# Kernel optimization log

Hardware: AMD Instinct MI355X
Metric: run time of the kernel (lower is better)

## Reference

```python
import jax, jax.numpy as jnp
import numpy as np

B, S, D_MODEL = 2, 2048, 1024
H, D = 16, 64
D_INNER = H * D
EPS = 1e-5


def setup_inputs() -> dict:
    key = jax.random.key(0)
    ks = jax.random.split(key, 10)
    sc = 0.02
    return {
        "x": jax.random.normal(ks[0], (B, S, D_MODEL), dtype=jnp.float32),
        "Wq": jax.random.normal(ks[1], (D_MODEL, D_INNER), dtype=jnp.float32) * sc,
        "Wk": jax.random.normal(ks[2], (D_MODEL, D_INNER), dtype=jnp.float32) * sc,
        "Wv": jax.random.normal(ks[3], (D_MODEL, D_INNER), dtype=jnp.float32) * sc,
        "Wg": jax.random.normal(ks[4], (D_MODEL, D_INNER), dtype=jnp.float32) * sc,
        "Wa": jax.random.normal(ks[5], (D_MODEL, H), dtype=jnp.float32) * sc,
        "ba": jax.random.normal(ks[6], (H,), dtype=jnp.float32) * sc,
        "Wo": jax.random.normal(ks[7], (D_INNER, D_MODEL), dtype=jnp.float32) * sc,
        "gn_w": jnp.ones((D_INNER,), dtype=jnp.float32),
        "gn_b": jnp.zeros((D_INNER,), dtype=jnp.float32),
    }


def reference(x, Wq, Wk, Wv, Wg, Wa, ba, Wo, gn_w, gn_b):
    b, s, _ = x.shape
    # projections -> [B,H,S,D]
    q = jax.nn.silu(jnp.einsum('bsm,md->bsd', x, Wq).reshape(b, s, H, D).transpose(0, 2, 1, 3))
    k = jax.nn.silu(jnp.einsum('bsm,md->bsd', x, Wk).reshape(b, s, H, D).transpose(0, 2, 1, 3))
    v = jnp.einsum('bsm,md->bsd', x, Wv).reshape(b, s, H, D).transpose(0, 2, 1, 3)

    # data-dependent log forget gate, per head: [B,H,S]
    log_alpha = -jax.nn.softplus(jnp.einsum('bsm,mh->bsh', x, Wa) + ba)
    cum = jnp.cumsum(log_alpha, axis=1).transpose(0, 2, 1)  # [B,H,S]

    # decay[b,h,i,j] = exp(cum[i] - cum[j]) for j <= i, else 0
    diff = cum[:, :, :, None] - cum[:, :, None, :]  # [B,H,S,S]
    causal = jnp.tril(jnp.ones((s, s), dtype=bool))
    decay = jnp.exp(jnp.where(causal, diff, -jnp.inf))

    attn = jnp.einsum('bhid,bhjd->bhij', q, k) * decay
    o = jnp.einsum('bhij,bhjd->bhid', attn, v)  # [B,H,S,D]
    o = o.transpose(0, 2, 1, 3)  # [B,S,H,D]

    # GroupNorm(H groups) over channels-within-group and spatial dim S
    mean = jnp.mean(o, axis=(1, 3), keepdims=True)          # per (b,h)
    var = jnp.var(o, axis=(1, 3), keepdims=True)
    o = (o - mean) / jnp.sqrt(var + EPS)
    o = o * gn_w.reshape(H, D) + gn_b.reshape(H, D)
    o = o.reshape(b, s, H * D)

    gate = jax.nn.sigmoid(jnp.einsum('bsm,md->bsd', x, Wg))
    return jnp.einsum('bsd,dm->bsm', o * gate, Wo)
```

## Files before the change

kernel.cpp:

```cpp
#include <hip/hip_runtime.h>
#include <math.h>
#include <stdint.h>

typedef __attribute__((ext_vector_type(4))) float f32x4;
typedef __attribute__((ext_vector_type(8))) short bf16x8;

constexpr int NB = 2;
constexpr int NS = 2048;
constexpr int NM = 1024;
constexpr int NH = 16;
constexpr int ND = 64;
constexpr int NDI = 1024;

__device__ __forceinline__ float bf2f(unsigned short u) {
  uint32_t x = ((uint32_t)u) << 16; float f; __builtin_memcpy(&f, &x, 4); return f;
}
__device__ __forceinline__ unsigned short f2bf(float f) {
  uint32_t x; __builtin_memcpy(&x, &f, 4);
  x += 0x7FFFu + ((x >> 16) & 1u);
  return (unsigned short)(x >> 16);
}

__global__ __launch_bounds__(256) void k_prep(const float* __restrict__ x,
    const float* __restrict__ w0, const float* __restrict__ w1,
    const float* __restrict__ w2, const float* __restrict__ w3,
    const float* __restrict__ w4, const float* __restrict__ Wa,
    unsigned short* __restrict__ xb,
    unsigned short* __restrict__ t0, unsigned short* __restrict__ t1,
    unsigned short* __restrict__ t2, unsigned short* __restrict__ t3,
    unsigned short* __restrict__ t4, unsigned short* __restrict__ wa_pad) {
  int bid = blockIdx.x;
  if (bid < 2048) {
    int i = bid * 256 + threadIdx.x;
    const float4* p = (const float4*)(x + (size_t)i * 8);
    float4 a = p[0], b = p[1];
    unsigned short r[8] = {f2bf(a.x), f2bf(a.y), f2bf(a.z), f2bf(a.w),
                           f2bf(b.x), f2bf(b.y), f2bf(b.z), f2bf(b.w)};
    *(uint4*)(xb + (size_t)i * 8) = *(const uint4*)r;
  } else if (bid < 7168) {
    __shared__ float tile[32][33];
    int w = bid - 2048;
    int z = w >> 10, within = w & 1023;
    const float* src = z == 0 ? w0 : z == 1 ? w1 : z == 2 ? w2 : z == 3 ? w3 : w4;
    unsigned short* dst = z == 0 ? t0 : z == 1 ? t1 : z == 2 ? t2 : z == 3 ? t3 : t4;
    int c0 = (within & 31) * 32, r0 = (within >> 5) * 32;
    int tx = threadIdx.x & 31, ty = threadIdx.x >> 5;
    #pragma unroll
    for (int i = 0; i < 4; i++)
      tile[ty + i * 8][tx] = src[(size_t)(r0 + ty + i * 8) * 1024 + c0 + tx];
    __syncthreads();
    #pragma unroll
    for (int i = 0; i < 4; i++)
      dst[(size_t)(c0 + ty + i * 8) * 1024 + r0 + tx] = f2bf(tile[tx][ty + i * 8]);
  } else {
    int idx = (bid - 7168) * 256 + threadIdx.x;
    int h = idx >> 10, k2 = idx & 1023;
    wa_pad[idx] = (h < 16) ? f2bf(Wa[k2 * 16 + h]) : (unsigned short)0;
  }
}

__global__ __launch_bounds__(256) void k_la_gemm(const unsigned short* __restrict__ xb,
    const unsigned short* __restrict__ wa_pad, float* __restrict__ la4) {
  __shared__ unsigned short As[128 * 32];
  __shared__ unsigned short Bs[128 * 32];
  int tid = threadIdx.x;
  int row0 = blockIdx.y * 128;
  int kbeg = blockIdx.x * 256;
  float* Cp = la4 + (size_t)blockIdx.x * (32 * 2048);
  int w = tid >> 6, l = tid & 63;
  int wr = w >> 1, wc = w & 1;
  int lr = l & 15, lk = l >> 4;
  f32x4 acc[4] = {};
  for (int k0 = kbeg; k0 < kbeg + 256; k0 += 32) {
    __syncthreads();
    #pragma unroll
    for (int i = 0; i < 2; i++) {
      int idx = tid + i * 256;
      int r = idx >> 2, c = idx & 3;
      int cs = c ^ ((r >> 1) & 3);
      const unsigned short* srcA = xb + (size_t)(row0 + r) * NM + k0 + cs * 8;
      const unsigned short* srcB = wa_pad + (size_t)r * NM + k0 + cs * 8;
      __builtin_amdgcn_global_load_lds(
          (const __attribute__((address_space(1))) void*)srcA,
          (__attribute__((address_space(3))) void*)((char*)As + (w * 64 + i * 256) * 16),
          16, 0, 0);
      __builtin_amdgcn_global_load_lds(
          (const __attribute__((address_space(1))) void*)srcB,
          (__attribute__((address_space(3))) void*)((char*)Bs + (w * 64 + i * 256) * 16),
          16, 0, 0);
    }
    __syncthreads();
    if (wc == 0) {
      bf16x8 b = *(const bf16x8*)&Bs[lr * 32 + (lk ^ ((lr >> 1) & 3)) * 8];
      #pragma unroll
      for (int m = 0; m < 4; m++) {
        int ra = wr * 64 + m * 16 + lr;
        bf16x8 a = *(const bf16x8*)&As[ra * 32 + (lk ^ ((ra >> 1) & 3)) * 8];
        acc[m] = __builtin_amdgcn_mfma_f32_16x16x32_bf16(a, b, acc[m], 0, 0, 0);
      }
    }
  }
  if (wc == 0) {
    #pragma unroll
    for (int m = 0; m < 4; m++) {
      #pragma unroll
      for (int j = 0; j < 4; j++) {
        int row = row0 + wr * 64 + m * 16 + lk * 4 + j;
        int bb = row >> 11, s = row & 2047;
        Cp[((size_t)(bb * 16 + lr)) * 2048 + s] = acc[m][j];
      }
    }
  }
}

__global__ __launch_bounds__(256) void k_cumsum(const float* __restrict__ la4,
    const float* __restrict__ ba, float* __restrict__ cum,
    float* __restrict__ psum, float* __restrict__ psq) {
  int g = blockIdx.x;
  int h = g & 15;
  if (threadIdx.x == 0) { psum[g] = 0.f; psq[g] = 0.f; }
  float bah = ba[h];
  const float* p0 = la4 + (size_t)g * NS;
  float* out = cum + (size_t)g * NS;
  __shared__ float part[256];
  float v[8]; float sum = 0.f;
  int base = threadIdx.x * 8;
  #pragma unroll
  for (int i = 0; i < 8; i++) {
    int s = base + i;
    float z = p0[s] + p0[65536 + s] + p0[131072 + s] + p0[196608 + s] + bah;
    float sp = fmaxf(z, 0.f) + log1pf(expf(-fabsf(z)));
    v[i] = -sp; sum += v[i];
  }
  part[threadIdx.x] = sum;
  __syncthreads();
  for (int off = 1; off < 256; off <<= 1) {
    float add = (threadIdx.x >= off) ? part[threadIdx.x - off] : 0.f;
    __syncthreads();
    part[threadIdx.x] += add;
    __syncthreads();
  }
  float run = (threadIdx.x > 0) ? part[threadIdx.x - 1] : 0.f;
  #pragma unroll
  for (int i = 0; i < 8; i++) { run += v[i]; out[base + i] = run; }
}

__global__ __launch_bounds__(512, 2) void k_proj8(
    const unsigned short* __restrict__ A,
    const unsigned short* __restrict__ Wcat,
    unsigned short* __restrict__ q, unsigned short* __restrict__ k,
    unsigned short* __restrict__ v, unsigned short* __restrict__ g) {
  __shared__ unsigned short Ab[2][256 * 64];
  __shared__ unsigned short Bb[2][256 * 64];
  int tid = threadIdx.x;
  int bid = blockIdx.x;
  int wg = (bid & 7) * 32 + (bid >> 3);
  int bx = wg & 15, by = wg >> 4;
  int row0 = by * 256, col0 = bx * 256;
  int wid = tid >> 6, lane = tid & 63;
  int WR = wid >> 2, WC = wid & 3;
  int lr = lane & 15, lk = lane >> 4;

  auto stage = [&](int kt, int bi) {
    #pragma unroll
    for (int i = 0; i < 4; i++) {
      int idx = tid + i * 512;
      int r = idx >> 3, c = idx & 7;
      int cs = c ^ (r & 7);
      const unsigned short* srcA = A + (size_t)(row0 + r) * NM + kt * 64 + cs * 8;
      __builtin_amdgcn_global_load_lds(
          (const __attribute__((address_space(1))) void*)srcA,
          (__attribute__((address_space(3))) void*)((char*)&Ab[bi][0] + (wid * 64 + i * 512) * 16),
          16, 0, 0);
      const unsigned short* srcB = Wcat + (size_t)(col0 + r) * NM + kt * 64 + cs * 8;
      __builtin_amdgcn_global_load_lds(
          (const __attribute__((address_space(1))) void*)srcB,
          (__attribute__((address_space(3))) void*)((char*)&Bb[bi][0] + (wid * 64 + i * 512) * 16),
          16, 0, 0);
    }
  };

  stage(0, 0);
  stage(1, 1);

  f32x4 acc[8][4] = {};
  for (int kt = 0; kt < 16; ++kt) {
    int bi = kt & 1;
    if (kt < 15) asm volatile("s_waitcnt vmcnt(8)" ::: "memory");
    else         asm volatile("s_waitcnt vmcnt(0)" ::: "memory");
    __builtin_amdgcn_sched_barrier(0);
    __builtin_amdgcn_s_barrier();

    const char* Ap = (const char*)&Ab[bi][0];
    const char* Bp = (const char*)&Bb[bi][0];
    bf16x8 a0[8], b0[4], a1[8], b1[4];
    #pragma unroll
    for (int m = 0; m < 8; m++) {
      int r = WR * 128 + m * 16 + lr;
      a0[m] = *(const bf16x8*)(Ap + r * 128 + ((lk ^ (r & 7)) * 16));
    }
    #pragma unroll
    for (int n = 0; n < 4; n++) {
      int r = WC * 64 + n * 16 + lr;
      b0[n] = *(const bf16x8*)(Bp + r * 128 + ((lk ^ (r & 7)) * 16));
    }
    #pragma unroll
    for (int m = 0; m < 8; m++)
      #pragma unroll
      for (int n = 0; n < 4; n++)
        acc[m][n] = __builtin_amdgcn_mfma_f32_16x16x32_bf16(a0[m], b0[n], acc[m][n], 0, 0, 0);
    #pragma unroll
    for (int m = 0; m < 8; m++) {
      int r = WR * 128 + m * 16 + lr;
      a1[m] = *(const bf16x8*)(Ap + r * 128 + (((lk + 4) ^ (r & 7)) * 16));
    }
    #pragma unroll
    for (int n = 0; n < 4; n++) {
      int r = WC * 64 + n * 16 + lr;
      b1[n] = *(const bf16x8*)(Bp + r * 128 + (((lk + 4) ^ (r & 7)) * 16));
    }
    asm volatile("s_waitcnt lgkmcnt(0)" ::: "memory");
    __builtin_amdgcn_sched_barrier(0);
    __builtin_amdgcn_s_barrier();
    if (kt + 2 < 16) stage(kt + 2, bi);
    __builtin_amdgcn_s_setprio(1);
    #pragma unroll
    for (int m = 0; m < 8; m++)
      #pragma unroll
      for (int n = 0; n < 4; n++)
        acc[m][n] = __builtin_amdgcn_mfma_f32_16x16x32_bf16(a1[m], b1[n], acc[m][n], 0, 0, 0);
    __builtin_amdgcn_s_setprio(0);
  }

  #pragma unroll
  for (int m = 0; m < 8; m++) {
    #pragma unroll
    for (int n = 0; n < 4; n++) {
      int col = col0 + WC * 64 + n * 16 + lr;
      int zone = col >> 10;
      unsigned short* dst = zone == 0 ? q : zone == 1 ? k : zone == 2 ? v : g;
      int cb = col & 1023;
      #pragma unroll
      for (int j = 0; j < 4; j++) {
        int row = row0 + WR * 128 + m * 16 + lk * 4 + j;
        float val = acc[m][n][j];
        if (zone <= 1) val = val / (1.f + expf(-val));
        else if (zone == 3) val = 1.f / (1.f + expf(-val));
        dst[(size_t)row * 1024 + cb] = f2bf(val);
      }
    }
  }
}

__global__ __launch_bounds__(256) void k_out2(const unsigned short* __restrict__ A,
    const unsigned short* __restrict__ Bt, float* __restrict__ C) {
  __shared__ unsigned short As[2][128 * 64];
  __shared__ unsigned short Bs[2][128 * 64];
  int tid = threadIdx.x;
  int bid = blockIdx.x;
  int wg = (bid & 7) * 32 + (bid >> 3);
  int bx = wg & 7, by = wg >> 3;
  int row0 = by * 128, col0 = bx * 128;
  int w = tid >> 6, l = tid & 63;
  int wr = w >> 1, wc = w & 1;
  int lr = l & 15, lk = l >> 4;

  auto stage = [&](int t, int bi) {
    #pragma unroll
    for (int i = 0; i < 4; i++) {
      int idx = tid + i * 256;
      int r = idx >> 3, c = idx & 7;
      int cs = c ^ (r & 7);
      const unsigned short* srcA = A + (size_t)(row0 + r) * NM + t * 64 + cs * 8;
      __builtin_amdgcn_global_load_lds(
          (const __attribute__((address_space(1))) void*)srcA,
          (__attribute__((address_space(3))) void*)((char*)&As[bi][0] + idx * 16),
          16, 0, 0);
      const unsigned short* srcB = Bt + (size_t)(col0 + r) * NM + t * 64 + cs * 8;
      __builtin_amdgcn_global_load_lds(
          (const __attribute__((address_space(1))) void*)srcB,
          (__attribute__((address_space(3))) void*)((char*)&Bs[bi][0] + idx * 16),
          16, 0, 0);
    }
  };

  stage(0, 0);
  asm volatile("s_waitcnt vmcnt(0)" ::: "memory");
  __builtin_amdgcn_s_barrier();

  f32x4 acc[4][4] = {};
  int cur = 0;
  for (int t = 0; t < 16; ++t) {
    if (t < 15) stage(t + 1, cur ^ 1);
    const char* Ap = (const char*)&As[cur][0];
    const char* Bp = (const char*)&Bs[cur][0];
    bf16x8 a[4][2], b[4][2];
    #pragma unroll
    for (int m = 0; m < 4; m++) {
      int ra = wr * 64 + m * 16 + lr;
      #pragma unroll
      for (int kk = 0; kk < 2; kk++)
        a[m][kk] = *(const bf16x8*)(Ap + ra * 128 + (((kk * 4 + lk) ^ (ra & 7)) * 16));
    }
    #pragma unroll
    for (int n = 0; n < 4; n++) {
      int rb = wc * 64 + n * 16 + lr;
      #pragma unroll
      for (int kk = 0; kk < 2; kk++)
        b[n][kk] = *(const bf16x8*)(Bp + rb * 128 + (((kk * 4 + lk) ^ (rb & 7)) * 16));
    }
    __builtin_amdgcn_s_setprio(1);
    #pragma unroll
    for (int kk = 0; kk < 2; kk++)
      #pragma unroll
      for (int m = 0; m < 4; m++)
        #pragma unroll
        for (int n = 0; n < 4; n++)
          acc[m][n] = __builtin_amdgcn_mfma_f32_16x16x32_bf16(a[m][kk], b[n][kk], acc[m][n], 0, 0, 0);
    __builtin_amdgcn_s_setprio(0);
    asm volatile("s_waitcnt vmcnt(0)" ::: "memory");
    __builtin_amdgcn_s_barrier();
    cur ^= 1;
  }
  #pragma unroll
  for (int m = 0; m < 4; m++)
    #pragma unroll
    for (int n = 0; n < 4; n++)
      #pragma unroll
      for (int j = 0; j < 4; j++) {
        int row = row0 + wr * 64 + m * 16 + lk * 4 + j;
        int col = col0 + wc * 64 + n * 16 + lr;
        C[(size_t)row * NM + col] = acc[m][n][j];
      }
}

__global__ __launch_bounds__(256) void k_attn(const unsigned short* __restrict__ q,
    const unsigned short* __restrict__ kk, const unsigned short* __restrict__ vv,
    const float* __restrict__ cum, unsigned short* __restrict__ o,
    float* __restrict__ psum, float* __restrict__ psq) {
  int it = blockIdx.x, h = blockIdx.y, b = blockIdx.z;
  int i0 = it * 64;
  __shared__ unsigned short Qs[64 * 64];
  __shared__ unsigned short Ks[64 * 64];
  __shared__ unsigned short Ps[64 * 64];
  __shared__ unsigned short Vs[64 * 66];
  __shared__ float ci[64], cj[64];
  __shared__ int jlo_s;
  int tid = threadIdx.x;
  int w = tid >> 6, lane = tid & 63;
  int cl = lane & 15, hi = lane >> 4;
  const size_t hb = (size_t)b * NS * NDI + (size_t)h * ND;
  const float* cumh = cum + (size_t)(b * NH + h) * NS;

  #pragma unroll
  for (int lp = 0; lp < 2; lp++) {
    int idx = tid + lp * 256;
    int r = idx >> 3, cb = (idx & 7) * 16;
    uint4 t = *(const uint4*)(q + hb + (size_t)(i0 + r) * NDI + (cb >> 1));
    *(uint4*)((char*)Qs + r * 128 + (cb ^ ((r & 7) << 4))) = t;
  }
  if (tid < 64) ci[tid] = cumh[i0 + tid];
  if (tid < 64) {
    int jt = tid;
    bool ok = (jt <= it) && (cumh[i0] - cumh[jt * 64 + 63] >= -25.f);
    unsigned long long mask = __ballot(ok);
    if (tid == 0) jlo_s = (int)__builtin_ctzll(mask);
  }
  __syncthreads();
  int jlo = jlo_s;

  int arow = w * 16 + cl;
  int xr = (cl & 7) << 4;
  const char* Qb = (const char*)Qs + arow * 128;
  const char* Pb = (const char*)Ps + arow * 128;
  f32x4 acco[4] = {};

  for (int jt = jlo; jt <= it; jt++) {
    int j0 = jt * 64;
    __syncthreads();
    if (tid < 64) cj[tid] = cumh[j0 + tid];
    __syncthreads();
    #pragma unroll
    for (int lp = 0; lp < 2; lp++) {
      int idx = tid + lp * 256;
      int r = idx >> 3, cb = (idx & 7) * 16;
      uint4 t = *(const uint4*)(kk + hb + (size_t)(j0 + r) * NDI + (cb >> 1));
      *(uint4*)((char*)Ks + r * 128 + (cb ^ ((r & 7) << 4))) = t;
      uint4 tv = *(const uint4*)(vv + hb + (size_t)(j0 + r) * NDI + (cb >> 1));
      unsigned int uv[4]; *(uint4*)uv = tv;
      unsigned int* vd = (unsigned int*)(Vs + r * 66 + (cb >> 1));
      vd[0] = uv[0]; vd[1] = uv[1]; vd[2] = uv[2]; vd[3] = uv[3];
    }
    __syncthreads();
    bf16x8 a0 = *(const bf16x8*)(Qb + ((hi * 16) ^ xr));
    bf16x8 a1 = *(const bf16x8*)(Qb + ((64 + hi * 16) ^ xr));
    f32x4 accs[4] = {};
    #pragma unroll
    for (int jtile = 0; jtile < 4; jtile++) {
      const char* Kb = (const char*)Ks + (jtile * 16 + cl) * 128;
      bf16x8 b0 = *(const bf16x8*)(Kb + ((hi * 16) ^ xr));
      bf16x8 b1 = *(const bf16x8*)(Kb + ((64 + hi * 16) ^ xr));
      accs[jtile] = __builtin_amdgcn_mfma_f32_16x16x32_bf16(a0, b0, accs[jtile], 0, 0, 0);
      accs[jtile] = __builtin_amdgcn_mfma_f32_16x16x32_bf16(a1, b1, accs[jtile], 0, 0, 0);
    }
    #pragma unroll
    for (int jtile = 0; jtile < 4; jtile++) {
      #pragma unroll
      for (int reg = 0; reg < 4; reg++) {
        int irl = w * 16 + hi * 4 + reg;
        int jl = jtile * 16 + cl;
        float dec = ((j0 + jl) <= (i0 + irl)) ? __expf(ci[irl] - cj[jl]) : 0.f;
        float pv = accs[jtile][reg] * dec;
        *(unsigned short*)((char*)Ps + irl * 128 + ((2 * jl) ^ ((irl & 7) << 4))) = f2bf(pv);
      }
    }
    __syncthreads();
    #pragma unroll
    for (int kk2 = 0; kk2 < 2; kk2++) {
      bf16x8 pa = *(const bf16x8*)(Pb + ((kk2 * 64 + hi * 16) ^ xr));
      #pragma unroll
      for (int dt = 0; dt < 4; dt++) {
        bf16x8 vb;
        #pragma unroll
        for (int e = 0; e < 8; e++)
          vb[e] = (short)Vs[(kk2 * 32 + hi * 8 + e) * 66 + dt * 16 + cl];
        acco[dt] = __builtin_amdgcn_mfma_f32_16x16x32_bf16(pa, vb, acco[dt], 0, 0, 0);
      }
    }
  }
  #pragma unroll
  for (int dt = 0; dt < 4; dt++) {
    #pragma unroll
    for (int reg = 0; reg < 4; reg++) {
      int row = i0 + w * 16 + hi * 4 + reg;
      o[hb + (size_t)row * NDI + dt * 16 + cl] = f2bf(acco[dt][reg]);
    }
  }
  __syncthreads();
  float* ls = (float*)Ps;
  float* lq = ls + 256;
  float sm = 0.f, sq = 0.f;
  #pragma unroll
  for (int dt = 0; dt < 4; dt++)
    #pragma unroll
    for (int reg = 0; reg < 4; reg++) { float t2 = acco[dt][reg]; sm += t2; sq += t2 * t2; }
  ls[tid] = sm; lq[tid] = sq;
  __syncthreads();
  for (int off = 128; off > 0; off >>= 1) {
    if (tid < off) { ls[tid] += ls[tid + off]; lq[tid] += lq[tid + off]; }
    __syncthreads();
  }
  if (tid == 0) {
    atomicAdd(&psum[b * NH + h], ls[0]);
    atomicAdd(&psq[b * NH + h], lq[0]);
  }
}

__global__ __launch_bounds__(256) void k_gate(const unsigned short* __restrict__ o,
    const unsigned short* __restrict__ gsig, const float* __restrict__ psum,
    const float* __restrict__ psq, const float* __restrict__ gnw,
    const float* __restrict__ gnb, unsigned short* __restrict__ u) {
  int idx4 = blockIdx.x * 256 + threadIdx.x;
  size_t base = (size_t)idx4 * 4;
  int c = (int)(base & (NDI - 1));
  int row = (int)(base >> 10);
  int b = row >> 11;
  int h = c >> 6;
  int g = b * NH + h;
  float n = (float)(NS * ND);
  float mean = psum[g] / n;
  float var = psq[g] / n - mean * mean;
  float rstd = rsqrtf(var + 1e-5f);
  ushort4 ov = *(const ushort4*)(o + base);
  ushort4 gv = *(const ushort4*)(gsig + base);
  float4 w4 = *(const float4*)(gnw + c);
  float4 b4 = *(const float4*)(gnb + c);
  unsigned short r[4];
  r[0] = f2bf(((bf2f(ov.x) - mean) * rstd * w4.x + b4.x) * bf2f(gv.x));
  r[1] = f2bf(((bf2f(ov.y) - mean) * rstd * w4.y + b4.y) * bf2f(gv.y));
  r[2] = f2bf(((bf2f(ov.z) - mean) * rstd * w4.z + b4.z) * bf2f(gv.z));
  r[3] = f2bf(((bf2f(ov.w) - mean) * rstd * w4.w + b4.w) * bf2f(gv.w));
  *(ushort4*)(u + base) = *(const ushort4*)r;
}

extern "C" void kernel_launch(void* const* d_in, const int* in_sizes, int n_in,
                              void* d_out, int out_size, void* d_ws, size_t ws_size,
                              hipStream_t stream) {
  const float* x   = (const float*)d_in[0];
  const float* Wq  = (const float*)d_in[1];
  const float* Wk  = (const float*)d_in[2];
  const float* Wv  = (const float*)d_in[3];
  const float* Wg  = (const float*)d_in[4];
  const float* Wa  = (const float*)d_in[5];
  const float* ba  = (const float*)d_in[6];
  const float* Wo  = (const float*)d_in[7];
  const float* gnw = (const float*)d_in[8];
  const float* gnb = (const float*)d_in[9];
  float* out = (float*)d_out;

  const size_t NTOK = (size_t)NB * NS;
  char* p = (char*)d_ws;
  float* la4 = (float*)p;                 p += (size_t)4 * 32 * NS * 4;
  float* cum = (float*)p;                 p += (size_t)NB * NH * NS * 4;
  float* psum = (float*)p;                p += 32 * 4;
  float* psq  = (float*)p;                p += 32 * 4;
  p = (char*)(((uintptr_t)p + 255) & ~(uintptr_t)255);
  unsigned short* xb   = (unsigned short*)p; p += NTOK * NM * 2;
  unsigned short* Wcat = (unsigned short*)p; p += (size_t)4 * NM * NDI * 2;
  unsigned short* wto  = (unsigned short*)p; p += (size_t)NDI * NM * 2;
  unsigned short* wa_pad = (unsigned short*)p; p += (size_t)128 * NM * 2;
  unsigned short* q  = (unsigned short*)p;  p += NTOK * NDI * 2;
  unsigned short* k  = (unsigned short*)p;  p += NTOK * NDI * 2;
  unsigned short* v  = (unsigned short*)p;  p += NTOK * NDI * 2;
  unsigned short* g  = (unsigned short*)p;  p += NTOK * NDI * 2;
  unsigned short* u  = (unsigned short*)p;  p += NTOK * NDI * 2;
  unsigned short* o  = (unsigned short*)p;  p += NTOK * NDI * 2;

  unsigned short* wtq = Wcat;
  unsigned short* wtk = Wcat + (size_t)NM * NDI;
  unsigned short* wtv = Wcat + (size_t)2 * NM * NDI;
  unsigned short* wtg = Wcat + (size_t)3 * NM * NDI;

  k_prep    <<<dim3(7680), 256, 0, stream>>>(x, Wq, Wk, Wv, Wg, Wo, Wa,
                                             xb, wtq, wtk, wtv, wtg, wto, wa_pad);
  k_la_gemm <<<dim3(4, 32), 256, 0, stream>>>(xb, wa_pad, la4);
  k_cumsum  <<<dim3(NB * NH), 256, 0, stream>>>(la4, ba, cum, psum, psq);
  k_proj8   <<<dim3(256), 512, 0, stream>>>(xb, Wcat, q, k, v, g);
  k_attn    <<<dim3(32, NH, NB), 256, 0, stream>>>(q, k, v, cum, o, psum, psq);
  k_gate    <<<dim3(4096), 256, 0, stream>>>(o, g, psum, psq, gnw, gnb, u);
  k_out2    <<<dim3(256), 256, 0, stream>>>(u, wto, out);
}
```

Baseline: 123.6 us.

## Transpose V tile in LDS for vector B-operand loads; widen la GEMM split-K

The attention kernel now writes V into shared memory transposed, with D as rows and keys as columns. Each lane can then fetch its MFMA B operand as four 32-bit LDS reads instead of eight strided 16-bit gathers, at the price of scattered 16-bit stores when filling the tile. Separately, the log-alpha GEMM's split-K factor goes from 4 to 8, giving 256 blocks instead of 128 for more parallelism. The cumsum kernel then sums eight partial slices instead of four, and the workspace for the partials is doubled.

```diff
diff --git a/kernel.cpp b/kernel.cpp
--- a/kernel.cpp
+++ b/kernel.cpp
@@ -60,18 +60,18 @@
 }
 
 __global__ __launch_bounds__(256) void k_la_gemm(const unsigned short* __restrict__ xb,
-    const unsigned short* __restrict__ wa_pad, float* __restrict__ la4) {
+    const unsigned short* __restrict__ wa_pad, float* __restrict__ la8) {
   __shared__ unsigned short As[128 * 32];
   __shared__ unsigned short Bs[128 * 32];
   int tid = threadIdx.x;
   int row0 = blockIdx.y * 128;
-  int kbeg = blockIdx.x * 256;
-  float* Cp = la4 + (size_t)blockIdx.x * (32 * 2048);
+  int kbeg = blockIdx.x * 128;
+  float* Cp = la8 + (size_t)blockIdx.x * (32 * 2048);
   int w = tid >> 6, l = tid & 63;
   int wr = w >> 1, wc = w & 1;
   int lr = l & 15, lk = l >> 4;
   f32x4 acc[4] = {};
-  for (int k0 = kbeg; k0 < kbeg + 256; k0 += 32) {
+  for (int k0 = kbeg; k0 < kbeg + 128; k0 += 32) {
     __syncthreads();
     #pragma unroll
     for (int i = 0; i < 2; i++) {
@@ -113,14 +113,14 @@
   }
 }
 
-__global__ __launch_bounds__(256) void k_cumsum(const float* __restrict__ la4,
+__global__ __launch_bounds__(256) void k_cumsum(const float* __restrict__ la8,
     const float* __restrict__ ba, float* __restrict__ cum,
     float* __restrict__ psum, float* __restrict__ psq) {
   int g = blockIdx.x;
   int h = g & 15;
   if (threadIdx.x == 0) { psum[g] = 0.f; psq[g] = 0.f; }
   float bah = ba[h];
-  const float* p0 = la4 + (size_t)g * NS;
+  const float* p0 = la8 + (size_t)g * NS;
   float* out = cum + (size_t)g * NS;
   __shared__ float part[256];
   float v[8]; float sum = 0.f;
@@ -128,7 +128,9 @@
   #pragma unroll
   for (int i = 0; i < 8; i++) {
     int s = base + i;
-    float z = p0[s] + p0[65536 + s] + p0[131072 + s] + p0[196608 + s] + bah;
+    float z = bah;
+    #pragma unroll
+    for (int sl = 0; sl < 8; sl++) z += p0[sl * 65536 + s];
     float sp = fmaxf(z, 0.f) + log1pf(expf(-fabsf(z)));
     v[i] = -sp; sum += v[i];
   }
@@ -343,7 +345,7 @@
   __shared__ unsigned short Qs[64 * 64];
   __shared__ unsigned short Ks[64 * 64];
   __shared__ unsigned short Ps[64 * 64];
-  __shared__ unsigned short Vs[64 * 66];
+  __shared__ unsigned short Vt[64 * 66];
   __shared__ float ci[64], cj[64];
   __shared__ int jlo_s;
   int tid = threadIdx.x;
@@ -387,9 +389,10 @@
       uint4 t = *(const uint4*)(kk + hb + (size_t)(j0 + r) * NDI + (cb >> 1));
       *(uint4*)((char*)Ks + r * 128 + (cb ^ ((r & 7) << 4))) = t;
       uint4 tv = *(const uint4*)(vv + hb + (size_t)(j0 + r) * NDI + (cb >> 1));
-      unsigned int uv[4]; *(uint4*)uv = tv;
-      unsigned int* vd = (unsigned int*)(Vs + r * 66 + (cb >> 1));
-      vd[0] = uv[0]; vd[1] = uv[1]; vd[2] = uv[2]; vd[3] = uv[3];
+      unsigned short us[8]; *(uint4*)us = tv;
+      int c8 = (idx & 7) * 8;
+      #pragma unroll
+      for (int e = 0; e < 8; e++) Vt[(c8 + e) * 66 + r] = us[e];
     }
     __syncthreads();
     bf16x8 a0 = *(const bf16x8*)(Qb + ((hi * 16) ^ xr));
@@ -420,10 +423,10 @@
       bf16x8 pa = *(const bf16x8*)(Pb + ((kk2 * 64 + hi * 16) ^ xr));
       #pragma unroll
       for (int dt = 0; dt < 4; dt++) {
-        bf16x8 vb;
-        #pragma unroll
-        for (int e = 0; e < 8; e++)
-          vb[e] = (short)Vs[(kk2 * 32 + hi * 8 + e) * 66 + dt * 16 + cl];
+        const unsigned int* vp = (const unsigned int*)(Vt + (dt * 16 + cl) * 66 + kk2 * 32 + hi * 8);
+        uint4 tmp;
+        tmp.x = vp[0]; tmp.y = vp[1]; tmp.z = vp[2]; tmp.w = vp[3];
+        bf16x8 vb = *(const bf16x8*)&tmp;
         acco[dt] = __builtin_amdgcn_mfma_f32_16x16x32_bf16(pa, vb, acco[dt], 0, 0, 0);
       }
     }
@@ -500,7 +503,7 @@
 
   const size_t NTOK = (size_t)NB * NS;
   char* p = (char*)d_ws;
-  float* la4 = (float*)p;                 p += (size_t)4 * 32 * NS * 4;
+  float* la8 = (float*)p;                 p += (size_t)8 * 32 * NS * 4;
   float* cum = (float*)p;                 p += (size_t)NB * NH * NS * 4;
   float* psum = (float*)p;                p += 32 * 4;
   float* psq  = (float*)p;                p += 32 * 4;
@@ -523,8 +526,8 @@
 
   k_prep    <<<dim3(7680), 256, 0, stream>>>(x, Wq, Wk, Wv, Wg, Wo, Wa,
                                              xb, wtq, wtk, wtv, wtg, wto, wa_pad);
-  k_la_gemm <<<dim3(4, 32), 256, 0, stream>>>(xb, wa_pad, la4);
-  k_cumsum  <<<dim3(NB * NH), 256, 0, stream>>>(la4, ba, cum, psum, psq);
+  k_la_gemm <<<dim3(8, 32), 256, 0, stream>>>(xb, wa_pad, la8);
+  k_cumsum  <<<dim3(NB * NH), 256, 0, stream>>>(la8, ba, cum, psum, psq);
   k_proj8   <<<dim3(256), 512, 0, stream>>>(xb, Wcat, q, k, v, g);
   k_attn    <<<dim3(32, NH, NB), 256, 0, stream>>>(q, k, v, cum, o, psum, psq);
   k_gate    <<<dim3(4096), 256, 0, stream>>>(o, g, psum, psq, gnw, gnb, u);
```

New measurement: 121.6 us. About the same (-1.6%).
